# Kernel optimization log

Measured on AMD Instinct MI355X. Metric: run time of the kernel, lower is better.

Reference implementation:

```python
import jax, jax.numpy as jnp
import numpy as np
import math

F = 64        # num_features (multiplicity of each irrep)
N = 16000     # nodes
E = 256000    # edges (avg_num_neighbors = 16)
S = 4         # num_species
DE = 32       # scalar edge feature dim (radial basis)
W = 128       # interaction_mlp_width
AVG_NEIGH = 16.0
SQ2 = math.sqrt(2.0)
SQ3 = math.sqrt(3.0)


def setup_inputs() -> dict:
    key = jax.random.key(0)
    ks = jax.random.split(key, 32)
    def nrm(k, shape, scale=1.0):
        return jax.random.normal(k, shape, dtype=jnp.float32) * scale
    inp = {}
    # forward args
    inp["vectors"] = nrm(ks[0], (E, 1, 3))
    inp["lengths"] = jax.random.uniform(ks[1], (E, 1), dtype=jnp.float32)
    inp["node_s"] = nrm(ks[2], (N, F))            # 64x0e part of node_feats
    inp["node_v"] = nrm(ks[3], (N, F, 3))         # 64x1o part of node_feats
    inp["scalar_edge_feats"] = nrm(ks[4], (E, DE))
    inp["node_specie"] = jax.random.randint(ks[5], (N,), 0, S)
    inp["senders"] = jax.random.randint(ks[6], (E,), 0, N)
    inp["receivers"] = jax.random.randint(ks[7], (E,), 0, N)
    # parameters (e3nn Linear = per-irrep channel mixing, fan-in normalized; bias only on 0e)
    inp["W_up_s"] = nrm(ks[8], (F, F), F ** -0.5); inp["b_up_s"] = jnp.zeros((F,), jnp.float32)
    inp["W_up_v"] = nrm(ks[9], (F, F), F ** -0.5)
    din = 2 * F + DE + 1
    inp["mlp_W1"] = nrm(ks[10], (din, W), din ** -0.5); inp["mlp_b1"] = jnp.zeros((W,), jnp.float32)
    inp["mlp_W2"] = nrm(ks[11], (W, W), W ** -0.5); inp["mlp_b2"] = jnp.zeros((W,), jnp.float32)
    inp["mlp_W3"] = nrm(ks[12], (W, 3 * F), W ** -0.5); inp["mlp_b3"] = jnp.zeros((3 * F,), jnp.float32)
    inp["W_dn_s"] = nrm(ks[13], (F, F), F ** -0.5); inp["b_dn_s"] = jnp.zeros((F,), jnp.float32)
    inp["W_dn_v"] = nrm(ks[14], (2 * F, F), (2 * F) ** -0.5)
    # symmetric contraction weights (per species, per channel); correlation=2
    inp["w_sc_s"] = nrm(ks[15], (S, 3, F), 3 ** -0.5)   # paths to 0e: x0, x0^2, (x1.x1)/sqrt3
    inp["w_sc_v"] = nrm(ks[16], (S, 2, F), 2 ** -0.5)   # paths to 1o: x1, x0*x1
    inp["W_pb_s"] = nrm(ks[17], (F, F), F ** -0.5); inp["b_pb_s"] = jnp.zeros((F,), jnp.float32)
    inp["W_pb_v"] = nrm(ks[18], (F, F), F ** -0.5)
    inp["W_r1_s"] = nrm(ks[19], (F, 2 * F), F ** -0.5); inp["b_r1_s"] = jnp.zeros((2 * F,), jnp.float32)
    inp["W_r1_v"] = nrm(ks[20], (F, F), F ** -0.5)
    inp["W_r2_s"] = nrm(ks[21], (F, 1), F ** -0.5); inp["b_r2"] = jnp.zeros((1,), jnp.float32)
    inp["W_r2_v"] = nrm(ks[22], (F, 1), F ** -0.5)
    return inp


def reference(vectors, lengths, node_s, node_v, scalar_edge_feats, node_specie,
              senders, receivers,
              W_up_s, b_up_s, W_up_v,
              mlp_W1, mlp_b1, mlp_W2, mlp_b2, mlp_W3, mlp_b3,
              W_dn_s, b_dn_s, W_dn_v,
              w_sc_s, w_sc_v, W_pb_s, b_pb_s, W_pb_v,
              W_r1_s, b_r1_s, W_r1_v, W_r2_s, b_r2, W_r2_v):
    n = node_s.shape[0]
    # --- spherical harmonics, sh_irreps='1o', component normalization, normalize=False ---
    edge_v = SQ3 * vectors[:, 0, :]                              # [E,3]

    # --- InteractionBlock: linear_up ---
    h_s = node_s @ W_up_s + b_up_s                               # [N,F]
    h_v = jnp.einsum('nfi,fg->ngi', node_v, W_up_v)              # [N,F,3]

    # --- MessagePassingConvolution ---
    m_s = h_s[senders]                                           # [E,F] 0e
    m_v = h_v[senders]                                           # [E,F,3] 1o
    # tensor product with edge 1o, filtered to 0e+1o (unitary CG):
    tp_s = jnp.einsum('efi,ei->ef', m_v, edge_v) / SQ3           # 1o x 1o -> 0e  [E,F]
    tp_v1 = m_s[:, :, None] * edge_v[:, None, :]                 # 0e x 1o -> 1o  [E,F,3]
    tp_v2 = jnp.cross(m_v, edge_v[:, None, :]) / SQ2             # 1o x 1o -> 1o  [E,F,3]
    # scalar MLP mix (one scalar weight per output irrep = 3F)
    mlp_in = jnp.concatenate([m_s, h_s[receivers], scalar_edge_feats, lengths], axis=1)
    h = jax.nn.silu(mlp_in @ mlp_W1 + mlp_b1)
    h = jax.nn.silu(h @ mlp_W2 + mlp_b2)
    mix = h @ mlp_W3 + mlp_b3                                    # [E,3F]
    mix_s, mix_v1, mix_v2 = mix[:, :F], mix[:, F:2 * F], mix[:, 2 * F:]
    tp_s = tp_s * mix_s
    tp_v = jnp.concatenate([tp_v1 * mix_v1[:, :, None], tp_v2 * mix_v2[:, :, None]], axis=1)  # [E,2F,3]
    # scatter-add to receivers, normalize by avg_num_neighbors
    agg_s = jax.ops.segment_sum(tp_s, receivers, num_segments=n) / AVG_NEIGH   # [N,F]
    agg_v = jax.ops.segment_sum(tp_v, receivers, num_segments=n) / AVG_NEIGH   # [N,2F,3]
    # linear_down
    f_s = agg_s @ W_dn_s + b_dn_s                                # [N,F]
    f_v = jnp.einsum('nfi,fg->ngi', agg_v, W_dn_v)               # [N,F,3]

    # --- EquivariantProductBasisBlock: symmetric contraction (correlation=2), per-species ---
    ws = w_sc_s[node_specie]                                     # [N,3,F]
    wv = w_sc_v[node_specie]                                     # [N,2,F]
    vv = jnp.sum(f_v * f_v, axis=-1) / SQ3                       # 1o (x) 1o -> 0e, symmetric
    sc_s = ws[:, 0] * f_s + ws[:, 1] * (f_s * f_s) + ws[:, 2] * vv           # [N,F]
    sc_v = wv[:, 0][:, :, None] * f_v + wv[:, 1][:, :, None] * (f_s[:, :, None] * f_v)  # [N,F,3]
    p_s = sc_s @ W_pb_s + b_pb_s                                 # node_feats 0e out
    p_v = jnp.einsum('nfi,fg->ngi', sc_v, W_pb_v)                # node_feats 1o out

    # --- NonLinearReadoutBlock: linear to (2F x 0e + F x 1o), gate, linear to 1x0e+1x1o ---
    r_s = p_s @ W_r1_s + b_r1_s                                  # [N,2F]
    r_v = jnp.einsum('nfi,fg->ngi', p_v, W_r1_v)                 # [N,F,3]
    act = jax.nn.silu(r_s[:, :F])
    gates = jax.nn.silu(r_s[:, F:])
    g_v = gates[:, :, None] * r_v                                # gated vectors
    out_s = act @ W_r2_s + b_r2                                  # [N,1]  0e output
    out_v = jnp.einsum('nfi,fo->noi', g_v, W_r2_v)               # [N,1,3] 1o output
    return out_s, out_v, p_s, p_v
```

## Files before the change

### kernel.cpp

```cpp
#include <hip/hip_runtime.h>

typedef short bf16x8 __attribute__((ext_vector_type(8)));
typedef float f32x4  __attribute__((ext_vector_type(4)));
typedef unsigned short ushort_t;

__device__ __forceinline__ float silu(float x) {
    float t = __expf(-x);
    return x * __builtin_amdgcn_rcpf(1.f + t);
}

__device__ __forceinline__ ushort_t f2bs(float x) {
    union { float f; unsigned int u; } v; v.f = x;
    unsigned int r = v.u + 0x7FFF + ((v.u >> 16) & 1);
    return (ushort_t)(r >> 16);
}
__device__ __forceinline__ ushort_t f2bs_t(float x) {
    union { float f; unsigned int u; } v; v.f = x;
    return (ushort_t)(v.u >> 16);
}
__device__ __forceinline__ float bs2f(ushort_t x) {
    union { unsigned int u; float f; } v; v.u = ((unsigned int)x) << 16; return v.f;
}

constexpr int N_   = 16000;
constexpr int E_   = 256000;
constexpr int Fd   = 64;

constexpr float SQ3f    = 1.7320508075688772f;
constexpr float INV_SQ3 = 0.5773502691896258f;
constexpr float INV_SQ2 = 0.7071067811865476f;
constexpr float INV_AVG = 0.0625f;

constexpr int OFF_OS = 0;
constexpr int OFF_OV = N_;
constexpr int OFF_PS = OFF_OV + 3 * N_;
constexpr int OFF_PV = OFF_PS + N_ * Fd;

constexpr int W1P_SZ = 6 * 8 * 512;
constexpr int W2P_SZ = 4 * 8 * 512;
constexpr int W3P_SZ = 4 * 12 * 512;

constexpr int AGG_W = 448;

__global__ __launch_bounds__(256) void pack_kernel(
    const float* __restrict__ W1, const float* __restrict__ W2,
    const float* __restrict__ W3,
    ushort_t* __restrict__ W1p, ushort_t* __restrict__ W2p,
    ushort_t* __restrict__ W3p)
{
    int idx = blockIdx.x * 256 + threadIdx.x;
    if (idx < W1P_SZ) {
        int j = idx & 7, lane = (idx >> 3) & 63, tile = idx >> 9;
        int c = tile >> 3, t = tile & 7;
        int k = c * 32 + (lane >> 4) * 8 + j;
        int n = t * 16 + (lane & 15);
        W1p[idx] = f2bs(k < 161 ? W1[k * 128 + n] : 0.f);
    } else if (idx < W1P_SZ + W2P_SZ) {
        int q = idx - W1P_SZ;
        int j = q & 7, lane = (q >> 3) & 63, tile = q >> 9;
        int c = tile >> 3, t = tile & 7;
        int k = c * 32 + (lane >> 4) * 8 + j;
        int n = t * 16 + (lane & 15);
        W2p[q] = f2bs(W2[k * 128 + n]);
    } else {
        int q = idx - W1P_SZ - W2P_SZ;
        int j = q & 7, lane = (q >> 3) & 63, tile = q >> 9;
        int c = tile / 12, t = tile % 12;
        int k = c * 32 + (lane >> 4) * 8 + j;
        int n = t * 16 + (lane & 15);
        W3p[q] = f2bs(W3[k * 192 + n]);
    }
}

__global__ __launch_bounds__(64, 4) void up_kernel(
    const float* __restrict__ node_s, const float* __restrict__ node_v,
    const float* __restrict__ W_up_s, const float* __restrict__ b_up_s,
    const float* __restrict__ W_up_v,
    const int* __restrict__ receivers, int* __restrict__ cnt,
    ushort_t* __restrict__ hs_bf, float* __restrict__ h_v)
{
    __shared__ float ns[4][64];
    __shared__ float nv[4][64][3];
    const int n0 = blockIdx.x * 4;
    const int g  = threadIdx.x;

    {
        int e = blockIdx.x * 64 + g;
        atomicAdd(&cnt[receivers[e]], 1);
    }

    #pragma unroll
    for (int j = 0; j < 4; j++) ns[j][g] = node_s[(n0 + j) * 64 + g];
    for (int idx = g; idx < 4 * 192; idx += 64) {
        int j = idx / 192, r = idx - j * 192;
        nv[j][r / 3][r % 3] = node_v[(size_t)n0 * 192 + idx];
    }
    __syncthreads();

    float as[4], a0[4], a1[4], a2[4];
    float bb = b_up_s[g];
    #pragma unroll
    for (int j = 0; j < 4; j++) { as[j] = bb; a0[j] = a1[j] = a2[j] = 0.f; }
    #pragma unroll 4
    for (int f = 0; f < 64; f++) {
        float wss = W_up_s[f * 64 + g];
        float wv  = W_up_v[f * 64 + g];
        #pragma unroll
        for (int j = 0; j < 4; j++) {
            as[j] += ns[j][f] * wss;
            a0[j] += nv[j][f][0] * wv;
            a1[j] += nv[j][f][1] * wv;
            a2[j] += nv[j][f][2] * wv;
        }
    }
    #pragma unroll
    for (int j = 0; j < 4; j++) {
        hs_bf[(n0 + j) * 64 + g] = f2bs(as[j]);
        h_v[(n0 + j) * 192 + 0 * 64 + g] = a0[j];
        h_v[(n0 + j) * 192 + 1 * 64 + g] = a1[j];
        h_v[(n0 + j) * 192 + 2 * 64 + g] = a2[j];
    }
}

__global__ __launch_bounds__(1024) void scan_kernel(
    const int* __restrict__ cnt, int* __restrict__ base, int* __restrict__ cursor)
{
    __shared__ int part[1024];
    const int t = threadIdx.x;
    int v[16];
    int s = 0;
    if (t < 1000) {
        const int4* c4 = (const int4*)(cnt + t * 16);
        #pragma unroll
        for (int q = 0; q < 4; q++) {
            int4 w = c4[q];
            v[q * 4 + 0] = w.x; v[q * 4 + 1] = w.y;
            v[q * 4 + 2] = w.z; v[q * 4 + 3] = w.w;
            s += w.x + w.y + w.z + w.w;
        }
    }
    part[t] = s;
    __syncthreads();
    for (int off = 1; off < 1024; off <<= 1) {
        int u = (t >= off) ? part[t - off] : 0;
        __syncthreads();
        part[t] += u;
        __syncthreads();
    }
    if (t < 1000) {
        int run = part[t] - s;
        int b[16];
        #pragma unroll
        for (int i = 0; i < 16; i++) { b[i] = run; run += v[i]; }
        int4* bb = (int4*)(base + t * 16);
        int4* cc = (int4*)(cursor + t * 16);
        #pragma unroll
        for (int q = 0; q < 4; q++) {
            int4 w = { b[q * 4], b[q * 4 + 1], b[q * 4 + 2], b[q * 4 + 3] };
            bb[q] = w;
            cc[q] = w;
        }
    }
}

__global__ __launch_bounds__(256) void perm_kernel(
    const int* __restrict__ receivers, int* __restrict__ cursor,
    int* __restrict__ eid)
{
    int e = blockIdx.x * 256 + threadIdx.x;
    int r = receivers[e];
    int p = atomicAdd(&cursor[r], 1);
    eid[p] = e;
}

__global__ __launch_bounds__(256, 3) void edge_mlp_kernel(
    const float* __restrict__ lengths, const float* __restrict__ sef,
    const int* __restrict__ senders, const int* __restrict__ receivers,
    const float* __restrict__ vectors, const int* __restrict__ eid,
    const float* __restrict__ b1f, const float* __restrict__ b2f,
    const float* __restrict__ b3f,
    const ushort_t* __restrict__ hs_bf, const float* __restrict__ h_v,
    const ushort_t* __restrict__ W1p, const ushort_t* __restrict__ W2p,
    const ushort_t* __restrict__ W3p,
    float* __restrict__ agg)
{
    __shared__ ushort_t Als[64 * 200];
    __shared__ ushort_t Hs[64 * 136];
    __shared__ int snd_s[64];
    __shared__ int rcv_s[64];
    __shared__ float ev_s[64][3];

    const int tid  = threadIdx.x;
    const int wave = tid >> 6, lane = tid & 63;
    const int quad = lane >> 4, l4 = lane & 15;
    const int e0   = blockIdx.x * 64;

    if (tid < 64) {
        int e = eid[e0 + tid];
        snd_s[tid] = senders[e];
        rcv_s[tid] = receivers[e];
        ev_s[tid][0] = SQ3f * vectors[e * 3 + 0];
        ev_s[tid][1] = SQ3f * vectors[e * 3 + 1];
        ev_s[tid][2] = SQ3f * vectors[e * 3 + 2];
    }

    {
        const int e  = tid & 63;
        const int ge = eid[e0 + e];
        const int snd = senders[ge];
        const int rcv = receivers[ge];
        for (int c = tid >> 6; c < 24; c += 4) {
            bf16x8 v;
            if (c < 8) {
                v = *(const bf16x8*)(hs_bf + snd * 64 + c * 8);
            } else if (c < 16) {
                v = *(const bf16x8*)(hs_bf + rcv * 64 + (c - 8) * 8);
            } else if (c < 20) {
                const float4 s0 = *(const float4*)(sef + (size_t)ge * 32 + (c - 16) * 8);
                const float4 s1 = *(const float4*)(sef + (size_t)ge * 32 + (c - 16) * 8 + 4);
                v[0] = (short)f2bs(s0.x); v[1] = (short)f2bs(s0.y);
                v[2] = (short)f2bs(s0.z); v[3] = (short)f2bs(s0.w);
                v[4] = (short)f2bs(s1.x); v[5] = (short)f2bs(s1.y);
                v[6] = (short)f2bs(s1.z); v[7] = (short)f2bs(s1.w);
            } else if (c == 20) {
                v = (bf16x8){0,0,0,0,0,0,0,0};
                v[0] = (short)f2bs(lengths[ge]);
            } else {
                v = (bf16x8){0,0,0,0,0,0,0,0};
            }
            *(bf16x8*)(&Als[e * 200 + c * 8]) = v;
        }
    }
    __syncthreads();

    const bf16x8* B1 = (const bf16x8*)W1p;
    const bf16x8* B2 = (const bf16x8*)W2p;
    const bf16x8* B3 = (const bf16x8*)W3p;

    {
        f32x4 acc[2][4];
        #pragma unroll
        for (int ti = 0; ti < 2; ti++)
            #pragma unroll
            for (int m = 0; m < 4; m++) acc[ti][m] = (f32x4){0,0,0,0};
        #pragma unroll
        for (int c = 0; c < 6; c++) {
            bf16x8 b0 = B1[(c * 8 + wave * 2 + 0) * 64 + lane];
            bf16x8 b1 = B1[(c * 8 + wave * 2 + 1) * 64 + lane];
            #pragma unroll
            for (int m = 0; m < 4; m++) {
                bf16x8 a = *(const bf16x8*)(&Als[(m * 16 + l4) * 200 + c * 32 + quad * 8]);
                acc[0][m] = __builtin_amdgcn_mfma_f32_16x16x32_bf16(a, b0, acc[0][m], 0, 0, 0);
                acc[1][m] = __builtin_amdgcn_mfma_f32_16x16x32_bf16(a, b1, acc[1][m], 0, 0, 0);
            }
        }
        #pragma unroll
        for (int ti = 0; ti < 2; ti++) {
            int t = wave * 2 + ti;
            float bb = b1f[t * 16 + l4];
            #pragma unroll
            for (int m = 0; m < 4; m++)
                #pragma unroll
                for (int r = 0; r < 4; r++)
                    Hs[(m * 16 + quad * 4 + r) * 136 + t * 16 + l4] =
                        f2bs_t(silu(acc[ti][m][r] + bb));
        }
    }
    __syncthreads();

    {
        f32x4 acc[2][4];
        #pragma unroll
        for (int ti = 0; ti < 2; ti++)
            #pragma unroll
            for (int m = 0; m < 4; m++) acc[ti][m] = (f32x4){0,0,0,0};
        #pragma unroll
        for (int c = 0; c < 4; c++) {
            bf16x8 b0 = B2[(c * 8 + wave * 2 + 0) * 64 + lane];
            bf16x8 b1 = B2[(c * 8 + wave * 2 + 1) * 64 + lane];
            #pragma unroll
            for (int m = 0; m < 4; m++) {
                bf16x8 a = *(const bf16x8*)(&Hs[(m * 16 + l4) * 136 + c * 32 + quad * 8]);
                acc[0][m] = __builtin_amdgcn_mfma_f32_16x16x32_bf16(a, b0, acc[0][m], 0, 0, 0);
                acc[1][m] = __builtin_amdgcn_mfma_f32_16x16x32_bf16(a, b1, acc[1][m], 0, 0, 0);
            }
        }
        #pragma unroll
        for (int ti = 0; ti < 2; ti++) {
            int t = wave * 2 + ti;
            float bb = b2f[t * 16 + l4];
            #pragma unroll
            for (int m = 0; m < 4; m++)
                #pragma unroll
                for (int r = 0; r < 4; r++)
                    Als[(m * 16 + quad * 4 + r) * 136 + t * 16 + l4] =
                        f2bs_t(silu(acc[ti][m][r] + bb));
        }
    }
    __syncthreads();

    {
        f32x4 acc[3][4];
        #pragma unroll
        for (int ti = 0; ti < 3; ti++)
            #pragma unroll
            for (int m = 0; m < 4; m++) acc[ti][m] = (f32x4){0,0,0,0};
        #pragma unroll
        for (int c = 0; c < 4; c++) {
            bf16x8 b0 = B3[(c * 12 + wave * 3 + 0) * 64 + lane];
            bf16x8 b1 = B3[(c * 12 + wave * 3 + 1) * 64 + lane];
            bf16x8 b2 = B3[(c * 12 + wave * 3 + 2) * 64 + lane];
            #pragma unroll
            for (int m = 0; m < 4; m++) {
                bf16x8 a = *(const bf16x8*)(&Als[(m * 16 + l4) * 136 + c * 32 + quad * 8]);
                acc[0][m] = __builtin_amdgcn_mfma_f32_16x16x32_bf16(a, b0, acc[0][m], 0, 0, 0);
                acc[1][m] = __builtin_amdgcn_mfma_f32_16x16x32_bf16(a, b1, acc[1][m], 0, 0, 0);
                acc[2][m] = __builtin_amdgcn_mfma_f32_16x16x32_bf16(a, b2, acc[2][m], 0, 0, 0);
            }
        }
        __syncthreads();
        #pragma unroll
        for (int ti = 0; ti < 3; ti++) {
            int t = wave * 3 + ti;
            float bb = b3f[t * 16 + l4];
            #pragma unroll
            for (int m = 0; m < 4; m++)
                #pragma unroll
                for (int r = 0; r < 4; r++)
                    Als[(m * 16 + quad * 4 + r) * 200 + t * 16 + l4] =
                        f2bs(acc[ti][m][r] + bb);
        }
    }
    __syncthreads();

    {
        const int g  = lane;
        const int p0 = wave * 16;
        float acc0 = 0.f, acc1 = 0.f, acc2 = 0.f, acc3 = 0.f;
        float acc4 = 0.f, acc5 = 0.f, acc6 = 0.f;
        int cur = rcv_s[p0];

        for (int jj = 0; jj < 16; jj += 8) {
            float M0[8], M1[8], M2[8], MS[8];
            #pragma unroll
            for (int j = 0; j < 8; j++) {
                const int se = snd_s[p0 + jj + j];
                M0[j] = h_v[(size_t)se * 192 + 0 * 64 + g];
                M1[j] = h_v[(size_t)se * 192 + 1 * 64 + g];
                M2[j] = h_v[(size_t)se * 192 + 2 * 64 + g];
                MS[j] = bs2f(hs_bf[se * 64 + g]);
            }
            #pragma unroll
            for (int j = 0; j < 8; j++) {
                const int el = p0 + jj + j;
                const int r  = rcv_s[el];
                if (r != cur) {
                    float* a = agg + (size_t)cur * AGG_W + g;
                    atomicAdd(a +   0, acc0); atomicAdd(a +  64, acc1);
                    atomicAdd(a + 128, acc2); atomicAdd(a + 192, acc3);
                    atomicAdd(a + 256, acc4); atomicAdd(a + 320, acc5);
                    atomicAdd(a + 384, acc6);
                    acc0 = acc1 = acc2 = acc3 = acc4 = acc5 = acc6 = 0.f;
                    cur = r;
                }
                const float ev0 = ev_s[el][0], ev1 = ev_s[el][1], ev2 = ev_s[el][2];
                const float mixs  = bs2f(Als[el * 200 +   0 + g]);
                const float mixv1 = bs2f(Als[el * 200 +  64 + g]);
                const float mixv2 = bs2f(Als[el * 200 + 128 + g]);
                const float k = MS[j] * mixv1;
                acc0 += (M0[j] * ev0 + M1[j] * ev1 + M2[j] * ev2) * mixs;
                acc1 += k * ev0;
                acc2 += k * ev1;
                acc3 += k * ev2;
                acc4 += (M1[j] * ev2 - M2[j] * ev1) * mixv2;
                acc5 += (M2[j] * ev0 - M0[j] * ev2) * mixv2;
                acc6 += (M0[j] * ev1 - M1[j] * ev0) * mixv2;
            }
        }
        float* a = agg + (size_t)cur * AGG_W + g;
        atomicAdd(a +   0, acc0); atomicAdd(a +  64, acc1);
        atomicAdd(a + 128, acc2); atomicAdd(a + 192, acc3);
        atomicAdd(a + 256, acc4); atomicAdd(a + 320, acc5);
        atomicAdd(a + 384, acc6);
    }
}

__global__ __launch_bounds__(256, 2) void node_fused_kernel(
    const float* __restrict__ agg,
    const int* __restrict__ specie,
    const float* __restrict__ W_dn_s, const float* __restrict__ b_dn_s,
    const float* __restrict__ W_dn_v,
    const float* __restrict__ w_sc_s, const float* __restrict__ w_sc_v,
    const float* __restrict__ W_pb_s, const float* __restrict__ b_pb_s,
    const float* __restrict__ W_pb_v,
    const float* __restrict__ W_r1_s, const float* __restrict__ b_r1_s,
    const float* __restrict__ W_r1_v,
    const float* __restrict__ W_r2_s, const float* __restrict__ b_r2,
    const float* __restrict__ W_r2_v,
    float* __restrict__ out)
{
    __shared__ float as_l[4][64];
    __shared__ float av_l[4][128][3];
    __shared__ float scs[4][64];
    __shared__ float scv[4][64][3];
    __shared__ float ps_[4][64];
    __shared__ float pv_[4][64][3];

    const int tid = threadIdx.x;
    const int w   = tid >> 6;
    const int g   = tid & 63;
    const int n   = blockIdx.x * 4 + w;

    const float* ag = agg + (size_t)n * AGG_W;
    as_l[w][g]        = ag[g]       * (INV_SQ3 * INV_AVG);
    av_l[w][g][0]     = ag[ 64 + g] * INV_AVG;
    av_l[w][g][1]     = ag[128 + g] * INV_AVG;
    av_l[w][g][2]     = ag[192 + g] * INV_AVG;
    av_l[w][64 + g][0] = ag[256 + g] * (INV_SQ2 * INV_AVG);
    av_l[w][64 + g][1] = ag[320 + g] * (INV_SQ2 * INV_AVG);
    av_l[w][64 + g][2] = ag[384 + g] * (INV_SQ2 * INV_AVG);

    float f_s = b_dn_s[g];
    #pragma unroll 8
    for (int f = 0; f < 64; f++) f_s += as_l[w][f] * W_dn_s[f * 64 + g];
    float fv0 = 0.f, fv1 = 0.f, fv2 = 0.f;
    #pragma unroll 8
    for (int f = 0; f < 128; f++) {
        float wt = W_dn_v[f * 64 + g];
        fv0 += av_l[w][f][0] * wt;
        fv1 += av_l[w][f][1] * wt;
        fv2 += av_l[w][f][2] * wt;
    }

    float vv = (fv0 * fv0 + fv1 * fv1 + fv2 * fv2) * INV_SQ3;
    int sp = specie[n];
    float ws0 = w_sc_s[sp * 192 + 0 * 64 + g];
    float ws1 = w_sc_s[sp * 192 + 1 * 64 + g];
    float ws2 = w_sc_s[sp * 192 + 2 * 64 + g];
    float wv0 = w_sc_v[sp * 128 + 0 * 64 + g];
    float wv1 = w_sc_v[sp * 128 + 1 * 64 + g];
    float sc_s = ws0 * f_s + ws1 * f_s * f_s + ws2 * vv;
    float kv = wv0 + wv1 * f_s;
    scs[w][g] = sc_s;
    scv[w][g][0] = kv * fv0;
    scv[w][g][1] = kv * fv1;
    scv[w][g][2] = kv * fv2;

    float p_s = b_pb_s[g];
    float pv0 = 0.f, pv1 = 0.f, pv2 = 0.f;
    #pragma unroll 8
    for (int f = 0; f < 64; f++) {
        float wps = W_pb_s[f * 64 + g];
        p_s += scs[w][f] * wps;
        float wpv = W_pb_v[f * 64 + g];
        pv0 += scv[w][f][0] * wpv;
        pv1 += scv[w][f][1] * wpv;
        pv2 += scv[w][f][2] * wpv;
    }
    ps_[w][g] = p_s;
    pv_[w][g][0] = pv0; pv_[w][g][1] = pv1; pv_[w][g][2] = pv2;

    out[OFF_PS + n * 64 + g] = p_s;
    out[OFF_PV + (size_t)n * 192 + g * 3 + 0] = pv0;
    out[OFF_PV + (size_t)n * 192 + g * 3 + 1] = pv1;
    out[OFF_PV + (size_t)n * 192 + g * 3 + 2] = pv2;

    float r0 = b_r1_s[g];
    float r1 = b_r1_s[g + 64];
    float rv0 = 0.f, rv1 = 0.f, rv2 = 0.f;
    #pragma unroll 8
    for (int f = 0; f < 64; f++) {
        float p = ps_[w][f];
        r0 += p * W_r1_s[f * 128 + g];
        r1 += p * W_r1_s[f * 128 + g + 64];
        float wrv = W_r1_v[f * 64 + g];
        rv0 += pv_[w][f][0] * wrv;
        rv1 += pv_[w][f][1] * wrv;
        rv2 += pv_[w][f][2] * wrv;
    }
    float act  = silu(r0);
    float gate = silu(r1);
    float o_s = act * W_r2_s[g];
    float wr2v = W_r2_v[g];
    float ov0 = gate * rv0 * wr2v;
    float ov1 = gate * rv1 * wr2v;
    float ov2 = gate * rv2 * wr2v;

    #pragma unroll
    for (int off = 32; off > 0; off >>= 1) {
        o_s += __shfl_down(o_s, off);
        ov0 += __shfl_down(ov0, off);
        ov1 += __shfl_down(ov1, off);
        ov2 += __shfl_down(ov2, off);
    }
    if (g == 0) {
        out[OFF_OS + n] = o_s + b_r2[0];
        out[OFF_OV + n * 3 + 0] = ov0;
        out[OFF_OV + n * 3 + 1] = ov1;
        out[OFF_OV + n * 3 + 2] = ov2;
    }
}

extern "C" void kernel_launch(void* const* d_in, const int* in_sizes, int n_in,
                              void* d_out, int out_size, void* d_ws, size_t ws_size,
                              hipStream_t stream)
{
    const float* vectors  = (const float*)d_in[0];
    const float* lengths  = (const float*)d_in[1];
    const float* node_s   = (const float*)d_in[2];
    const float* node_v   = (const float*)d_in[3];
    const float* sef      = (const float*)d_in[4];
    const int*  specie    = (const int*)d_in[5];
    const int*  senders   = (const int*)d_in[6];
    const int*  receivers = (const int*)d_in[7];
    const float* W_up_s   = (const float*)d_in[8];
    const float* b_up_s   = (const float*)d_in[9];
    const float* W_up_v   = (const float*)d_in[10];
    const float* mlp_W1   = (const float*)d_in[11];
    const float* mlp_b1   = (const float*)d_in[12];
    const float* mlp_W2   = (const float*)d_in[13];
    const float* mlp_b2   = (const float*)d_in[14];
    const float* mlp_W3   = (const float*)d_in[15];
    const float* mlp_b3   = (const float*)d_in[16];
    const float* W_dn_s   = (const float*)d_in[17];
    const float* b_dn_s   = (const float*)d_in[18];
    const float* W_dn_v   = (const float*)d_in[19];
    const float* w_sc_s   = (const float*)d_in[20];
    const float* w_sc_v   = (const float*)d_in[21];
    const float* W_pb_s   = (const float*)d_in[22];
    const float* b_pb_s   = (const float*)d_in[23];
    const float* W_pb_v   = (const float*)d_in[24];
    const float* W_r1_s   = (const float*)d_in[25];
    const float* b_r1_s   = (const float*)d_in[26];
    const float* W_r1_v   = (const float*)d_in[27];
    const float* W_r2_s   = (const float*)d_in[28];
    const float* b_r2     = (const float*)d_in[29];
    const float* W_r2_v   = (const float*)d_in[30];

    float* h_v   = (float*)d_ws;
    float* agg   = h_v + (size_t)N_ * 192;
    ushort_t* hs_bf = (ushort_t*)(agg + (size_t)N_ * AGG_W);
    ushort_t* W1p   = hs_bf + (size_t)N_ * 64;
    ushort_t* W2p   = W1p + W1P_SZ;
    ushort_t* W3p   = W2p + W2P_SZ;
    int* eid        = (int*)((((size_t)(W3p + W3P_SZ)) + 15) & ~(size_t)15);
    int* cnt        = eid + E_;
    int* base       = cnt + N_;
    int* cursor     = base + N_;

    float* out = (float*)d_out;

    hipMemsetAsync(cnt, 0, N_ * sizeof(int), stream);
    hipMemsetAsync(agg, 0, (size_t)N_ * AGG_W * sizeof(float), stream);

    up_kernel<<<N_ / 4, 64, 0, stream>>>(node_s, node_v, W_up_s, b_up_s, W_up_v,
                                         receivers, cnt, hs_bf, h_v);
    pack_kernel<<<256, 256, 0, stream>>>(mlp_W1, mlp_W2, mlp_W3, W1p, W2p, W3p);
    scan_kernel<<<1, 1024, 0, stream>>>(cnt, base, cursor);
    perm_kernel<<<E_ / 256, 256, 0, stream>>>(receivers, cursor, eid);

    edge_mlp_kernel<<<E_ / 64, 256, 0, stream>>>(
        lengths, sef, senders, receivers, vectors, eid,
        mlp_b1, mlp_b2, mlp_b3,
        hs_bf, h_v, W1p, W2p, W3p, agg);

    node_fused_kernel<<<N_ / 4, 256, 0, stream>>>(
        agg, specie,
        W_dn_s, b_dn_s, W_dn_v, w_sc_s, w_sc_v,
        W_pb_s, b_pb_s, W_pb_v, W_r1_s, b_r1_s, W_r1_v,
        W_r2_s, b_r2, W_r2_v, out);
}
```

Baseline: 374.1 us.

## Merge edge-MLP LDS buffers, prefetch sender vectors early, raise occupancy

The separate Als and Hs shared buffers are merged into one union buffer with an offset region for the second hidden layer, cutting LDS per block so that four blocks per CU can fit instead of three. The sender's scalar features are reused from the gathered A tile rather than reloaded from global memory. The first half of the sender h_v gather is issued before the MLP matmuls so its latency overlaps MFMA work. Barriers are replaced with an explicit lgkmcnt wait plus s_barrier, and an extra barrier guards reuse of the merged buffer. The trade-off is higher register pressure from the prefetched values, which may cause spills under the tighter launch bound.

```diff
diff --git a/kernel.cpp b/kernel.cpp
--- a/kernel.cpp
+++ b/kernel.cpp
@@ -22,6 +22,11 @@
     union { unsigned int u; float f; } v; v.u = ((unsigned int)x) << 16; return v.f;
 }
 
+#define BAR_LGKM() do { \
+    asm volatile("s_waitcnt lgkmcnt(0)" ::: "memory"); \
+    __builtin_amdgcn_s_barrier(); \
+} while (0)
+
 constexpr int N_   = 16000;
 constexpr int E_   = 256000;
 constexpr int Fd   = 64;
@@ -41,6 +46,8 @@
 constexpr int W3P_SZ = 4 * 12 * 512;
 
 constexpr int AGG_W = 448;
+
+constexpr int H2_OFF = 8704;
 
 __global__ __launch_bounds__(256) void pack_kernel(
     const float* __restrict__ W1, const float* __restrict__ W2,
@@ -173,7 +180,7 @@
     eid[p] = e;
 }
 
-__global__ __launch_bounds__(256, 3) void edge_mlp_kernel(
+__global__ __launch_bounds__(256, 4) void edge_mlp_kernel(
     const float* __restrict__ lengths, const float* __restrict__ sef,
     const int* __restrict__ senders, const int* __restrict__ receivers,
     const float* __restrict__ vectors, const int* __restrict__ eid,
@@ -184,8 +191,7 @@
     const ushort_t* __restrict__ W3p,
     float* __restrict__ agg)
 {
-    __shared__ ushort_t Als[64 * 200];
-    __shared__ ushort_t Hs[64 * 136];
+    __shared__ ushort_t U[17408];
     __shared__ int snd_s[64];
     __shared__ int rcv_s[64];
     __shared__ float ev_s[64][3];
@@ -228,10 +234,30 @@
             } else {
                 v = (bf16x8){0,0,0,0,0,0,0,0};
             }
-            *(bf16x8*)(&Als[e * 200 + c * 8]) = v;
-        }
-    }
-    __syncthreads();
+            *(bf16x8*)(&U[e * 200 + c * 8]) = v;
+        }
+    }
+    BAR_LGKM();
+
+    const int g_  = lane;
+    const int p0_ = wave * 16;
+
+    float PSa[16];
+    #pragma unroll
+    for (int j = 0; j < 16; j++) PSa[j] = bs2f(U[(p0_ + j) * 200 + g_]);
+
+    float P0[8], P1[8], P2[8];
+    {
+        int seP[8];
+        #pragma unroll
+        for (int j = 0; j < 8; j++) seP[j] = snd_s[p0_ + j];
+        #pragma unroll
+        for (int j = 0; j < 8; j++) {
+            P0[j] = h_v[(size_t)seP[j] * 192 +   0 + g_];
+            P1[j] = h_v[(size_t)seP[j] * 192 +  64 + g_];
+            P2[j] = h_v[(size_t)seP[j] * 192 + 128 + g_];
+        }
+    }
 
     const bf16x8* B1 = (const bf16x8*)W1p;
     const bf16x8* B2 = (const bf16x8*)W2p;
@@ -249,11 +275,12 @@
             bf16x8 b1 = B1[(c * 8 + wave * 2 + 1) * 64 + lane];
             #pragma unroll
             for (int m = 0; m < 4; m++) {
-                bf16x8 a = *(const bf16x8*)(&Als[(m * 16 + l4) * 200 + c * 32 + quad * 8]);
+                bf16x8 a = *(const bf16x8*)(&U[(m * 16 + l4) * 200 + c * 32 + quad * 8]);
                 acc[0][m] = __builtin_amdgcn_mfma_f32_16x16x32_bf16(a, b0, acc[0][m], 0, 0, 0);
                 acc[1][m] = __builtin_amdgcn_mfma_f32_16x16x32_bf16(a, b1, acc[1][m], 0, 0, 0);
             }
         }
+        BAR_LGKM();
         #pragma unroll
         for (int ti = 0; ti < 2; ti++) {
             int t = wave * 2 + ti;
@@ -262,11 +289,11 @@
             for (int m = 0; m < 4; m++)
                 #pragma unroll
                 for (int r = 0; r < 4; r++)
-                    Hs[(m * 16 + quad * 4 + r) * 136 + t * 16 + l4] =
+                    U[(m * 16 + quad * 4 + r) * 136 + t * 16 + l4] =
                         f2bs_t(silu(acc[ti][m][r] + bb));
         }
     }
-    __syncthreads();
+    BAR_LGKM();
 
     {
         f32x4 acc[2][4];
@@ -280,7 +307,7 @@
             bf16x8 b1 = B2[(c * 8 + wave * 2 + 1) * 64 + lane];
             #pragma unroll
             for (int m = 0; m < 4; m++) {
-                bf16x8 a = *(const bf16x8*)(&Hs[(m * 16 + l4) * 136 + c * 32 + quad * 8]);
+                bf16x8 a = *(const bf16x8*)(&U[(m * 16 + l4) * 136 + c * 32 + quad * 8]);
                 acc[0][m] = __builtin_amdgcn_mfma_f32_16x16x32_bf16(a, b0, acc[0][m], 0, 0, 0);
                 acc[1][m] = __builtin_amdgcn_mfma_f32_16x16x32_bf16(a, b1, acc[1][m], 0, 0, 0);
             }
@@ -293,11 +320,11 @@
             for (int m = 0; m < 4; m++)
                 #pragma unroll
                 for (int r = 0; r < 4; r++)
-                    Als[(m * 16 + quad * 4 + r) * 136 + t * 16 + l4] =
+                    U[H2_OFF + (m * 16 + quad * 4 + r) * 136 + t * 16 + l4] =
                         f2bs_t(silu(acc[ti][m][r] + bb));
         }
     }
-    __syncthreads();
+    BAR_LGKM();
 
     {
         f32x4 acc[3][4];
@@ -312,13 +339,13 @@
             bf16x8 b2 = B3[(c * 12 + wave * 3 + 2) * 64 + lane];
             #pragma unroll
             for (int m = 0; m < 4; m++) {
-                bf16x8 a = *(const bf16x8*)(&Als[(m * 16 + l4) * 136 + c * 32 + quad * 8]);
+                bf16x8 a = *(const bf16x8*)(&U[H2_OFF + (m * 16 + l4) * 136 + c * 32 + quad * 8]);
                 acc[0][m] = __builtin_amdgcn_mfma_f32_16x16x32_bf16(a, b0, acc[0][m], 0, 0, 0);
                 acc[1][m] = __builtin_amdgcn_mfma_f32_16x16x32_bf16(a, b1, acc[1][m], 0, 0, 0);
                 acc[2][m] = __builtin_amdgcn_mfma_f32_16x16x32_bf16(a, b2, acc[2][m], 0, 0, 0);
             }
         }
-        __syncthreads();
+        BAR_LGKM();
         #pragma unroll
         for (int ti = 0; ti < 3; ti++) {
             int t = wave * 3 + ti;
@@ -327,55 +354,83 @@
             for (int m = 0; m < 4; m++)
                 #pragma unroll
                 for (int r = 0; r < 4; r++)
-                    Als[(m * 16 + quad * 4 + r) * 200 + t * 16 + l4] =
+                    U[(m * 16 + quad * 4 + r) * 200 + t * 16 + l4] =
                         f2bs(acc[ti][m][r] + bb);
         }
     }
-    __syncthreads();
+    BAR_LGKM();
 
     {
-        const int g  = lane;
-        const int p0 = wave * 16;
+        const int g  = g_;
+        const int p0 = p0_;
         float acc0 = 0.f, acc1 = 0.f, acc2 = 0.f, acc3 = 0.f;
         float acc4 = 0.f, acc5 = 0.f, acc6 = 0.f;
         int cur = rcv_s[p0];
 
-        for (int jj = 0; jj < 16; jj += 8) {
-            float M0[8], M1[8], M2[8], MS[8];
+        float Q0[8], Q1[8], Q2[8];
+        {
+            int seQ[8];
+            #pragma unroll
+            for (int j = 0; j < 8; j++) seQ[j] = snd_s[p0 + 8 + j];
             #pragma unroll
             for (int j = 0; j < 8; j++) {
-                const int se = snd_s[p0 + jj + j];
-                M0[j] = h_v[(size_t)se * 192 + 0 * 64 + g];
-                M1[j] = h_v[(size_t)se * 192 + 1 * 64 + g];
-                M2[j] = h_v[(size_t)se * 192 + 2 * 64 + g];
-                MS[j] = bs2f(hs_bf[se * 64 + g]);
+                Q0[j] = h_v[(size_t)seQ[j] * 192 +   0 + g];
+                Q1[j] = h_v[(size_t)seQ[j] * 192 +  64 + g];
+                Q2[j] = h_v[(size_t)seQ[j] * 192 + 128 + g];
             }
-            #pragma unroll
-            for (int j = 0; j < 8; j++) {
-                const int el = p0 + jj + j;
-                const int r  = rcv_s[el];
-                if (r != cur) {
-                    float* a = agg + (size_t)cur * AGG_W + g;
-                    atomicAdd(a +   0, acc0); atomicAdd(a +  64, acc1);
-                    atomicAdd(a + 128, acc2); atomicAdd(a + 192, acc3);
-                    atomicAdd(a + 256, acc4); atomicAdd(a + 320, acc5);
-                    atomicAdd(a + 384, acc6);
-                    acc0 = acc1 = acc2 = acc3 = acc4 = acc5 = acc6 = 0.f;
-                    cur = r;
-                }
-                const float ev0 = ev_s[el][0], ev1 = ev_s[el][1], ev2 = ev_s[el][2];
-                const float mixs  = bs2f(Als[el * 200 +   0 + g]);
-                const float mixv1 = bs2f(Als[el * 200 +  64 + g]);
-                const float mixv2 = bs2f(Als[el * 200 + 128 + g]);
-                const float k = MS[j] * mixv1;
-                acc0 += (M0[j] * ev0 + M1[j] * ev1 + M2[j] * ev2) * mixs;
-                acc1 += k * ev0;
-                acc2 += k * ev1;
-                acc3 += k * ev2;
-                acc4 += (M1[j] * ev2 - M2[j] * ev1) * mixv2;
-                acc5 += (M2[j] * ev0 - M0[j] * ev2) * mixv2;
-                acc6 += (M0[j] * ev1 - M1[j] * ev0) * mixv2;
+        }
+
+        #pragma unroll
+        for (int j = 0; j < 8; j++) {
+            const int el = p0 + j;
+            const int r  = rcv_s[el];
+            if (r != cur) {
+                float* a = agg + (size_t)cur * AGG_W + g;
+                atomicAdd(a +   0, acc0); atomicAdd(a +  64, acc1);
+                atomicAdd(a + 128, acc2); atomicAdd(a + 192, acc3);
+                atomicAdd(a + 256, acc4); atomicAdd(a + 320, acc5);
+                atomicAdd(a + 384, acc6);
+                acc0 = acc1 = acc2 = acc3 = acc4 = acc5 = acc6 = 0.f;
+                cur = r;
             }
+            const float ev0 = ev_s[el][0], ev1 = ev_s[el][1], ev2 = ev_s[el][2];
+            const float mixs  = bs2f(U[el * 200 +   0 + g]);
+            const float mixv1 = bs2f(U[el * 200 +  64 + g]);
+            const float mixv2 = bs2f(U[el * 200 + 128 + g]);
+            const float k = PSa[j] * mixv1;
+            acc0 += (P0[j] * ev0 + P1[j] * ev1 + P2[j] * ev2) * mixs;
+            acc1 += k * ev0;
+            acc2 += k * ev1;
+            acc3 += k * ev2;
+            acc4 += (P1[j] * ev2 - P2[j] * ev1) * mixv2;
+            acc5 += (P2[j] * ev0 - P0[j] * ev2) * mixv2;
+            acc6 += (P0[j] * ev1 - P1[j] * ev0) * mixv2;
+        }
+        #pragma unroll
+        for (int j = 0; j < 8; j++) {
+            const int el = p0 + 8 + j;
+            const int r  = rcv_s[el];
+            if (r != cur) {
+                float* a = agg + (size_t)cur * AGG_W + g;
+                atomicAdd(a +   0, acc0); atomicAdd(a +  64, acc1);
+                atomicAdd(a + 128, acc2); atomicAdd(a + 192, acc3);
+                atomicAdd(a + 256, acc4); atomicAdd(a + 320, acc5);
+                atomicAdd(a + 384, acc6);
+                acc0 = acc1 = acc2 = acc3 = acc4 = acc5 = acc6 = 0.f;
+                cur = r;
+            }
+            const float ev0 = ev_s[el][0], ev1 = ev_s[el][1], ev2 = ev_s[el][2];
+            const float mixs  = bs2f(U[el * 200 +   0 + g]);
+            const float mixv1 = bs2f(U[el * 200 +  64 + g]);
+            const float mixv2 = bs2f(U[el * 200 + 128 + g]);
+            const float k = PSa[8 + j] * mixv1;
+            acc0 += (Q0[j] * ev0 + Q1[j] * ev1 + Q2[j] * ev2) * mixs;
+            acc1 += k * ev0;
+            acc2 += k * ev1;
+            acc3 += k * ev2;
+            acc4 += (Q1[j] * ev2 - Q2[j] * ev1) * mixv2;
+            acc5 += (Q2[j] * ev0 - Q0[j] * ev2) * mixv2;
+            acc6 += (Q0[j] * ev1 - Q1[j] * ev0) * mixv2;
         }
         float* a = agg + (size_t)cur * AGG_W + g;
         atomicAdd(a +   0, acc0); atomicAdd(a +  64, acc1);
```

Result: slower. 391.1 us (+4.5%).

## Merge edge-MLP LDS buffers into one union and raise occupancy to four blocks

Applied to the files above, without the earlier changes.

Replaces the separate Als and Hs shared arrays with one 17408-element union buffer. The buffer is reused across MLP stages, which needs an extra barrier after the layer-1 MFMA reads before H1 overwrites the input tile. H2 is placed at an offset. Shrinking LDS per block lets launch bounds rise from 3 to 4 blocks per CU. Barriers become an explicit lgkmcnt wait plus s_barrier. This trades one extra barrier and a tighter register budget for more waves in flight to hide the gather and atomic latency.

```diff
diff --git a/kernel.cpp b/kernel.cpp
--- a/kernel.cpp
+++ b/kernel.cpp
@@ -22,6 +22,11 @@
     union { unsigned int u; float f; } v; v.u = ((unsigned int)x) << 16; return v.f;
 }
 
+#define BAR_LGKM() do { \
+    asm volatile("s_waitcnt lgkmcnt(0)" ::: "memory"); \
+    __builtin_amdgcn_s_barrier(); \
+} while (0)
+
 constexpr int N_   = 16000;
 constexpr int E_   = 256000;
 constexpr int Fd   = 64;
@@ -41,6 +46,8 @@
 constexpr int W3P_SZ = 4 * 12 * 512;
 
 constexpr int AGG_W = 448;
+
+constexpr int H2_OFF = 8704;
 
 __global__ __launch_bounds__(256) void pack_kernel(
     const float* __restrict__ W1, const float* __restrict__ W2,
@@ -173,7 +180,7 @@
     eid[p] = e;
 }
 
-__global__ __launch_bounds__(256, 3) void edge_mlp_kernel(
+__global__ __launch_bounds__(256, 4) void edge_mlp_kernel(
     const float* __restrict__ lengths, const float* __restrict__ sef,
     const int* __restrict__ senders, const int* __restrict__ receivers,
     const float* __restrict__ vectors, const int* __restrict__ eid,
@@ -184,8 +191,7 @@
     const ushort_t* __restrict__ W3p,
     float* __restrict__ agg)
 {
-    __shared__ ushort_t Als[64 * 200];
-    __shared__ ushort_t Hs[64 * 136];
+    __shared__ ushort_t U[17408];
     __shared__ int snd_s[64];
     __shared__ int rcv_s[64];
     __shared__ float ev_s[64][3];
@@ -228,10 +234,10 @@
             } else {
                 v = (bf16x8){0,0,0,0,0,0,0,0};
             }
-            *(bf16x8*)(&Als[e * 200 + c * 8]) = v;
-        }
-    }
-    __syncthreads();
+            *(bf16x8*)(&U[e * 200 + c * 8]) = v;
+        }
+    }
+    BAR_LGKM();
 
     const bf16x8* B1 = (const bf16x8*)W1p;
     const bf16x8* B2 = (const bf16x8*)W2p;
@@ -249,11 +255,12 @@
             bf16x8 b1 = B1[(c * 8 + wave * 2 + 1) * 64 + lane];
             #pragma unroll
             for (int m = 0; m < 4; m++) {
-                bf16x8 a = *(const bf16x8*)(&Als[(m * 16 + l4) * 200 + c * 32 + quad * 8]);
+                bf16x8 a = *(const bf16x8*)(&U[(m * 16 + l4) * 200 + c * 32 + quad * 8]);
                 acc[0][m] = __builtin_amdgcn_mfma_f32_16x16x32_bf16(a, b0, acc[0][m], 0, 0, 0);
                 acc[1][m] = __builtin_amdgcn_mfma_f32_16x16x32_bf16(a, b1, acc[1][m], 0, 0, 0);
             }
         }
+        BAR_LGKM();
         #pragma unroll
         for (int ti = 0; ti < 2; ti++) {
             int t = wave * 2 + ti;
@@ -262,11 +269,11 @@
             for (int m = 0; m < 4; m++)
                 #pragma unroll
                 for (int r = 0; r < 4; r++)
-                    Hs[(m * 16 + quad * 4 + r) * 136 + t * 16 + l4] =
+                    U[(m * 16 + quad * 4 + r) * 136 + t * 16 + l4] =
                         f2bs_t(silu(acc[ti][m][r] + bb));
         }
     }
-    __syncthreads();
+    BAR_LGKM();
 
     {
         f32x4 acc[2][4];
@@ -280,7 +287,7 @@
             bf16x8 b1 = B2[(c * 8 + wave * 2 + 1) * 64 + lane];
             #pragma unroll
             for (int m = 0; m < 4; m++) {
-                bf16x8 a = *(const bf16x8*)(&Hs[(m * 16 + l4) * 136 + c * 32 + quad * 8]);
+                bf16x8 a = *(const bf16x8*)(&U[(m * 16 + l4) * 136 + c * 32 + quad * 8]);
                 acc[0][m] = __builtin_amdgcn_mfma_f32_16x16x32_bf16(a, b0, acc[0][m], 0, 0, 0);
                 acc[1][m] = __builtin_amdgcn_mfma_f32_16x16x32_bf16(a, b1, acc[1][m], 0, 0, 0);
             }
@@ -293,11 +300,11 @@
             for (int m = 0; m < 4; m++)
                 #pragma unroll
                 for (int r = 0; r < 4; r++)
-                    Als[(m * 16 + quad * 4 + r) * 136 + t * 16 + l4] =
+                    U[H2_OFF + (m * 16 + quad * 4 + r) * 136 + t * 16 + l4] =
                         f2bs_t(silu(acc[ti][m][r] + bb));
         }
     }
-    __syncthreads();
+    BAR_LGKM();
 
     {
         f32x4 acc[3][4];
@@ -312,13 +319,13 @@
             bf16x8 b2 = B3[(c * 12 + wave * 3 + 2) * 64 + lane];
             #pragma unroll
             for (int m = 0; m < 4; m++) {
-                bf16x8 a = *(const bf16x8*)(&Als[(m * 16 + l4) * 136 + c * 32 + quad * 8]);
+                bf16x8 a = *(const bf16x8*)(&U[H2_OFF + (m * 16 + l4) * 136 + c * 32 + quad * 8]);
                 acc[0][m] = __builtin_amdgcn_mfma_f32_16x16x32_bf16(a, b0, acc[0][m], 0, 0, 0);
                 acc[1][m] = __builtin_amdgcn_mfma_f32_16x16x32_bf16(a, b1, acc[1][m], 0, 0, 0);
                 acc[2][m] = __builtin_amdgcn_mfma_f32_16x16x32_bf16(a, b2, acc[2][m], 0, 0, 0);
             }
         }
-        __syncthreads();
+        BAR_LGKM();
         #pragma unroll
         for (int ti = 0; ti < 3; ti++) {
             int t = wave * 3 + ti;
@@ -327,11 +334,11 @@
             for (int m = 0; m < 4; m++)
                 #pragma unroll
                 for (int r = 0; r < 4; r++)
-                    Als[(m * 16 + quad * 4 + r) * 200 + t * 16 + l4] =
+                    U[(m * 16 + quad * 4 + r) * 200 + t * 16 + l4] =
                         f2bs(acc[ti][m][r] + bb);
         }
     }
-    __syncthreads();
+    BAR_LGKM();
 
     {
         const int g  = lane;
@@ -364,9 +371,9 @@
                     cur = r;
                 }
                 const float ev0 = ev_s[el][0], ev1 = ev_s[el][1], ev2 = ev_s[el][2];
-                const float mixs  = bs2f(Als[el * 200 +   0 + g]);
-                const float mixv1 = bs2f(Als[el * 200 +  64 + g]);
-                const float mixv2 = bs2f(Als[el * 200 + 128 + g]);
+                const float mixs  = bs2f(U[el * 200 +   0 + g]);
+                const float mixv1 = bs2f(U[el * 200 +  64 + g]);
+                const float mixv2 = bs2f(U[el * 200 + 128 + g]);
                 const float k = MS[j] * mixv1;
                 acc0 += (M0[j] * ev0 + M1[j] * ev1 + M2[j] * ev2) * mixs;
                 acc1 += k * ev0;
```

Result: faster. 363.8 us (-2.8%).
